# Optimization experiments

Hardware: AMD Instinct MI355X
Metric: run time of the kernel (lower is better)

The kernel has to match this reference:

```python
import jax, jax.numpy as jnp
import numpy as np

B, SIZE_IN, SIZE_OUT = 16384, 256, 4096
NUM_QUANTILES = 32  # boundaries per column = NUM_QUANTILES - 1 = 31


def setup_inputs() -> dict:
    key = jax.random.key(0)
    k1, k2, k3, k4 = jax.random.split(key, 4)
    x = jax.random.normal(k1, (B, SIZE_IN), dtype=jnp.float32)
    weights = jax.random.normal(k2, (SIZE_OUT, SIZE_IN), dtype=jnp.float32) * (1.0 / np.sqrt(SIZE_IN))
    bound = 1.0 / np.sqrt(SIZE_IN)
    bias = jax.random.uniform(k3, (SIZE_OUT,), dtype=jnp.float32, minval=-bound, maxval=bound)
    # per-column quantile boundaries, sorted ascending along last axis
    q = jax.random.normal(k4, (SIZE_OUT, NUM_QUANTILES - 1), dtype=jnp.float32) * np.sqrt(SIZE_IN)
    quantiles = jnp.sort(q, axis=-1)
    return {"x": x, "weights": weights, "bias": bias, "quantiles": quantiles}


def reference(x, weights, bias, quantiles):
    # w_times_x: [B, size_out]
    wx = jnp.matmul(x, weights.T)
    # binarySearchQuantiles: first i with activation <= quantiles[col][i],
    # else len(quantiles[col]) => searchsorted(side='left') per column.
    # quantiles: [size_out, Q-1], wx column j searched against quantiles[j].
    indices = jax.vmap(
        lambda bounds, vals: jnp.searchsorted(bounds, vals, side="left"),
        in_axes=(0, 1), out_axes=1,
    )(quantiles, wx)  # [B, size_out] int32
    out = wx + bias  # broadcast bias over batch
    return out, indices.astype(jnp.float32)
```

## Files before the change

kernel.cpp:

```cpp
#include <hip/hip_runtime.h>


#define B_DIM 16384
#define K_DIM 256
#define N_DIM 4096
#define NQ 31
#define QCAP 2048
#define DELTA 1e-3f

typedef __bf16 bf16x8 __attribute__((ext_vector_type(8)));
typedef float f32x4 __attribute__((ext_vector_type(4)));
typedef unsigned short ushort8 __attribute__((ext_vector_type(8)));

typedef const __attribute__((address_space(1))) unsigned int gu32;
typedef __attribute__((address_space(3))) unsigned int lu32;

__global__ __launch_bounds__(256)
void split_pack(const float* __restrict__ X, const float* __restrict__ W,
                unsigned short* __restrict__ Xhi, unsigned short* __restrict__ Xmid,
                unsigned short* __restrict__ Whi, unsigned short* __restrict__ Wmid)
{
    const int b = blockIdx.x;
    const int tid = threadIdx.x;
    const int r = tid >> 1, ch = tid & 1;

    const float* src;
    unsigned short *dhi, *dmid;
    if (b < 1024) {
        const unsigned u = b;
        src = X + ((size_t)(u >> 3) * 128 + r) * K_DIM + (u & 7) * 32 + ch * 16;
        dhi = Xhi + (size_t)u * 4096; dmid = Xmid + (size_t)u * 4096;
    } else {
        const unsigned u = b - 1024;
        src = W + ((size_t)(u >> 3) * 128 + r) * K_DIM + (u & 7) * 32 + ch * 16;
        dhi = Whi + (size_t)u * 4096; dmid = Wmid + (size_t)u * 4096;
    }

    float4 v0 = *(const float4*)src;
    float4 v1 = *(const float4*)(src + 4);
    float4 v2 = *(const float4*)(src + 8);
    float4 v3 = *(const float4*)(src + 12);
    float xs[16] = {v0.x, v0.y, v0.z, v0.w, v1.x, v1.y, v1.z, v1.w,
                    v2.x, v2.y, v2.z, v2.w, v3.x, v3.y, v3.z, v3.w};
    ushort8 h[2], m[2];
#pragma unroll
    for (int j = 0; j < 16; ++j) {
        float x = xs[j];
        __bf16 hb = (__bf16)x;
        float hf = (float)hb;
        __bf16 mb = (__bf16)(x - hf);
        h[j >> 3][j & 7] = __builtin_bit_cast(unsigned short, hb);
        m[j >> 3][j & 7] = __builtin_bit_cast(unsigned short, mb);
    }
    const unsigned off = (unsigned)(ch * 2) * 1024u + (unsigned)r * 8u;
    *(ushort8*)(dhi + off)         = h[0];
    *(ushort8*)(dhi + off + 1024)  = h[1];
    *(ushort8*)(dmid + off)        = m[0];
    *(ushort8*)(dmid + off + 1024) = m[1];
}

__global__ __launch_bounds__(256)
void eidetic_mfma(const unsigned short* __restrict__ Xhi, const unsigned short* __restrict__ Xmid,
                  const unsigned short* __restrict__ Whi, const unsigned short* __restrict__ Wmid,
                  const float* __restrict__ X, const float* __restrict__ W,
                  const float* __restrict__ bias, const float* __restrict__ Q,
                  float* __restrict__ out, float* __restrict__ idxo)
{
    __shared__ unsigned char smem[65536];
    const int tid = threadIdx.x;
    const int lane = tid & 63;
    const int w = tid >> 6;
    const int wm = w >> 1, wn = w & 1;
    const int l15 = lane & 15, lg = lane >> 4;

    const int bid = blockIdx.x;
    const int swz = ((bid & 7) << 9) | (bid >> 3);
    const int mb = swz >> 5, nb = swz & 31;
    const int m0 = mb << 7, n0 = nb << 7;

    const unsigned short* sbase = (w == 0) ? Xhi : (w == 1) ? Xmid : (w == 2) ? Whi : Wmid;
    const int tb = (w < 2) ? mb : nb;
    const unsigned short* sp = sbase + (size_t)tb * 32768 + (size_t)lane * 8;
    const unsigned ldw = (unsigned)w * 8192u;

    const unsigned aoff = (unsigned)(lg * 128 + wm * 64 + l15) * 16u;
    const unsigned boff = 16384u + (unsigned)(lg * 128 + wn * 64 + l15) * 16u;

    f32x4 acc[4][4];
#pragma unroll
    for (int i = 0; i < 4; ++i)
#pragma unroll
        for (int j = 0; j < 4; ++j) acc[i][j] = (f32x4){0.f, 0.f, 0.f, 0.f};

#pragma unroll
    for (int i = 0; i < 8; ++i)
        __builtin_amdgcn_global_load_lds((gu32*)(sp + i * 512),
                                         (lu32*)(smem + ldw + i * 1024), 16, 0, 0);

    for (int ks = 0; ks < 8; ++ks) {
        __syncthreads();
        if (ks < 7) {
            const unsigned short* s = sp + (ks + 1) * 4096;
            const unsigned bufn = ((unsigned)(ks + 1) & 1u) * 32768u;
#pragma unroll
            for (int i = 0; i < 8; ++i)
                __builtin_amdgcn_global_load_lds((gu32*)(s + i * 512),
                                                 (lu32*)(smem + bufn + ldw + i * 1024), 16, 0, 0);
        }
        const unsigned buf = ((unsigned)ks & 1u) * 32768u;
        bf16x8 ah[4], am[4], bh[4], bm[4];
#pragma unroll
        for (int f = 0; f < 4; ++f) {
            ah[f] = *(const bf16x8*)(smem + buf + aoff + f * 256);
            am[f] = *(const bf16x8*)(smem + buf + 8192u + aoff + f * 256);
            bh[f] = *(const bf16x8*)(smem + buf + boff + f * 256);
            bm[f] = *(const bf16x8*)(smem + buf + 8192u + boff + f * 256);
        }
#pragma unroll
        for (int fi = 0; fi < 4; ++fi)
#pragma unroll
            for (int fj = 0; fj < 4; ++fj) {
                acc[fi][fj] = __builtin_amdgcn_mfma_f32_16x16x32_bf16(ah[fi], bh[fj], acc[fi][fj], 0, 0, 0);
                acc[fi][fj] = __builtin_amdgcn_mfma_f32_16x16x32_bf16(ah[fi], bm[fj], acc[fi][fj], 0, 0, 0);
                acc[fi][fj] = __builtin_amdgcn_mfma_f32_16x16x32_bf16(am[fi], bh[fj], acc[fi][fj], 0, 0, 0);
            }
    }

    float* Qs = (float*)smem;
    {
        const float* qsrc = Q + (size_t)n0 * NQ;
        for (int t = tid; t < 128 * NQ; t += 256) Qs[t] = qsrc[t];
    }
    int* qcnt = (int*)(smem + 15872);
    int* qbuf = qcnt + 1;
    if (tid == 0) *qcnt = 0;
    __syncthreads();

    const int rb = wm * 64 + (lg << 2);

    float bv4[4]; int qb4[4]; int ln4[4];
#pragma unroll
    for (int fj = 0; fj < 4; ++fj) {
        const int ln = wn * 64 + fj * 16 + l15;
        ln4[fj] = ln;
        bv4[fj] = bias[n0 + ln];
        qb4[fj] = ln * NQ;
    }

#pragma unroll
    for (int fi = 0; fi < 4; ++fi) {
#pragma unroll
        for (int r = 0; r < 4; ++r) {
            const int lrow = rb + fi * 16 + r;
            const size_t rowo = (size_t)(m0 + lrow) * N_DIM + n0;
            float ov[4], cv[4];
#pragma unroll
            for (int fj = 0; fj < 4; ++fj) {
                const float v = acc[fi][fj][r];
                const int qb = qb4[fj];
                int c = (Qs[qb + 15] < v) ? 16 : 0;
                c += (Qs[qb + c + 7] < v) ? 8 : 0;
                c += (Qs[qb + c + 3] < v) ? 4 : 0;
                c += (Qs[qb + c + 1] < v) ? 2 : 0;
                c += (Qs[qb + c] < v) ? 1 : 0;
                bool fl = false;
                if (c > 0)  fl = (v - Qs[qb + c - 1]) < DELTA;
                if (c < NQ) fl |= (Qs[qb + c] - v) < DELTA;
                if (fl) {
                    int slot = atomicAdd(qcnt, 1);
                    if (slot < QCAP) qbuf[slot] = (lrow << 7) | ln4[fj];
                }
                ov[fj] = v + bv4[fj];
                cv[fj] = (float)c;
            }
#pragma unroll
            for (int fj = 0; fj < 4; ++fj) out[rowo + ln4[fj]]  = ov[fj];
#pragma unroll
            for (int fj = 0; fj < 4; ++fj) idxo[rowo + ln4[fj]] = cv[fj];
        }
    }

    __syncthreads();
    int tot = *qcnt;
    if (tot > QCAP) tot = QCAP;
    for (int e = tid; e < tot; e += 256) {
        const int pk = qbuf[e];
        const int lm = pk >> 7, lc = pk & 127;
        const float* xr = X + (size_t)(m0 + lm) * K_DIM;
        const float* wr = W + (size_t)(n0 + lc) * K_DIM;
        float a = 0.f;
        for (int k = 0; k < K_DIM; ++k) a = fmaf(xr[k], wr[k], a);
        int c = 0;
        const int qb2 = lc * NQ;
        for (int t = 0; t < NQ; ++t) c += (Qs[qb2 + t] < a) ? 1 : 0;
        const size_t o = (size_t)(m0 + lm) * N_DIM + (n0 + lc);
        out[o] = a + bias[n0 + lc];
        idxo[o] = (float)c;
    }
}

extern "C" void kernel_launch(void* const* d_in, const int* in_sizes, int n_in,
                              void* d_out, int out_size, void* d_ws, size_t ws_size,
                              hipStream_t stream) {
    const float* x    = (const float*)d_in[0];
    const float* wgt  = (const float*)d_in[1];
    const float* bias = (const float*)d_in[2];
    const float* q    = (const float*)d_in[3];
    float* out  = (float*)d_out;
    float* idxo = out + (size_t)B_DIM * N_DIM;

    unsigned short* Xhi  = (unsigned short*)d_ws;
    unsigned short* Xmid = Xhi  + (size_t)B_DIM * K_DIM;
    unsigned short* Whi  = Xmid + (size_t)B_DIM * K_DIM;
    unsigned short* Wmid = Whi  + (size_t)N_DIM * K_DIM;

    hipLaunchKernelGGL(split_pack, dim3(1280), dim3(256), 0, stream,
                       x, wgt, Xhi, Xmid, Whi, Wmid);
    hipLaunchKernelGGL(eidetic_mfma, dim3(4096), dim3(256), 0, stream,
                       Xhi, Xmid, Whi, Wmid, x, wgt, bias, q, out, idxo);
}
```

Measured before the change: 789.3 us.

## Split 128x128 tile across 8 waves instead of 4 in MFMA kernel

Doubles the workgroup to 512 threads so each wave computes a 64x32 sub-tile instead of 64x64, and splits the global-to-LDS staging loads across two waves per operand plane. This halves per-wave accumulator registers and MFMA work, aiming for more waves in flight to hide memory latency during the K loop and the epilogue stores. In exchange, A fragments are reloaded from LDS by more waves, and the 64KB LDS per block still limits how many blocks fit per CU.

```diff
diff --git a/kernel.cpp b/kernel.cpp
--- a/kernel.cpp
+++ b/kernel.cpp
@@ -59,7 +59,7 @@
     *(ushort8*)(dmid + off + 1024) = m[1];
 }
 
-__global__ __launch_bounds__(256)
+__global__ __launch_bounds__(512, 4)
 void eidetic_mfma(const unsigned short* __restrict__ Xhi, const unsigned short* __restrict__ Xmid,
                   const unsigned short* __restrict__ Whi, const unsigned short* __restrict__ Wmid,
                   const float* __restrict__ X, const float* __restrict__ W,
@@ -70,7 +70,7 @@
     const int tid = threadIdx.x;
     const int lane = tid & 63;
     const int w = tid >> 6;
-    const int wm = w >> 1, wn = w & 1;
+    const int wm = w >> 2, wn = w & 3;
     const int l15 = lane & 15, lg = lane >> 4;
 
     const int bid = blockIdx.x;
@@ -78,22 +78,23 @@
     const int mb = swz >> 5, nb = swz & 31;
     const int m0 = mb << 7, n0 = nb << 7;
 
-    const unsigned short* sbase = (w == 0) ? Xhi : (w == 1) ? Xmid : (w == 2) ? Whi : Wmid;
-    const int tb = (w < 2) ? mb : nb;
-    const unsigned short* sp = sbase + (size_t)tb * 32768 + (size_t)lane * 8;
-    const unsigned ldw = (unsigned)w * 8192u;
-
-    const unsigned aoff = (unsigned)(lg * 128 + wm * 64 + l15) * 16u;
-    const unsigned boff = 16384u + (unsigned)(lg * 128 + wn * 64 + l15) * 16u;
-
-    f32x4 acc[4][4];
+    const int p = w >> 1, h = w & 1;
+    const unsigned short* sbase = (p == 0) ? Xhi : (p == 1) ? Xmid : (p == 2) ? Whi : Wmid;
+    const int tb = (p < 2) ? mb : nb;
+    const unsigned short* sp = sbase + (size_t)tb * 32768 + h * 2048 + (size_t)lane * 8;
+    const unsigned ldw = (unsigned)p * 8192u + (unsigned)h * 4096u;
+
+    const unsigned abase = (unsigned)(lg * 128 + wm * 64 + l15) * 16u;
+    const unsigned bbase = 16384u + (unsigned)(lg * 128 + wn * 32 + l15) * 16u;
+
+    f32x4 acc[4][2];
 #pragma unroll
     for (int i = 0; i < 4; ++i)
 #pragma unroll
-        for (int j = 0; j < 4; ++j) acc[i][j] = (f32x4){0.f, 0.f, 0.f, 0.f};
-
-#pragma unroll
-    for (int i = 0; i < 8; ++i)
+        for (int j = 0; j < 2; ++j) acc[i][j] = (f32x4){0.f, 0.f, 0.f, 0.f};
+
+#pragma unroll
+    for (int i = 0; i < 4; ++i)
         __builtin_amdgcn_global_load_lds((gu32*)(sp + i * 512),
                                          (lu32*)(smem + ldw + i * 1024), 16, 0, 0);
 
@@ -103,23 +104,26 @@
             const unsigned short* s = sp + (ks + 1) * 4096;
             const unsigned bufn = ((unsigned)(ks + 1) & 1u) * 32768u;
 #pragma unroll
-            for (int i = 0; i < 8; ++i)
+            for (int i = 0; i < 4; ++i)
                 __builtin_amdgcn_global_load_lds((gu32*)(s + i * 512),
                                                  (lu32*)(smem + bufn + ldw + i * 1024), 16, 0, 0);
         }
         const unsigned buf = ((unsigned)ks & 1u) * 32768u;
-        bf16x8 ah[4], am[4], bh[4], bm[4];
+        bf16x8 ah[4], am[4], bh[2], bm[2];
 #pragma unroll
         for (int f = 0; f < 4; ++f) {
-            ah[f] = *(const bf16x8*)(smem + buf + aoff + f * 256);
-            am[f] = *(const bf16x8*)(smem + buf + 8192u + aoff + f * 256);
-            bh[f] = *(const bf16x8*)(smem + buf + boff + f * 256);
-            bm[f] = *(const bf16x8*)(smem + buf + 8192u + boff + f * 256);
+            ah[f] = *(const bf16x8*)(smem + buf + abase + f * 256);
+            am[f] = *(const bf16x8*)(smem + buf + 8192u + abase + f * 256);
+        }
+#pragma unroll
+        for (int f = 0; f < 2; ++f) {
+            bh[f] = *(const bf16x8*)(smem + buf + bbase + f * 256);
+            bm[f] = *(const bf16x8*)(smem + buf + 8192u + bbase + f * 256);
         }
 #pragma unroll
         for (int fi = 0; fi < 4; ++fi)
 #pragma unroll
-            for (int fj = 0; fj < 4; ++fj) {
+            for (int fj = 0; fj < 2; ++fj) {
                 acc[fi][fj] = __builtin_amdgcn_mfma_f32_16x16x32_bf16(ah[fi], bh[fj], acc[fi][fj], 0, 0, 0);
                 acc[fi][fj] = __builtin_amdgcn_mfma_f32_16x16x32_bf16(ah[fi], bm[fj], acc[fi][fj], 0, 0, 0);
                 acc[fi][fj] = __builtin_amdgcn_mfma_f32_16x16x32_bf16(am[fi], bh[fj], acc[fi][fj], 0, 0, 0);
@@ -129,7 +133,7 @@
     float* Qs = (float*)smem;
     {
         const float* qsrc = Q + (size_t)n0 * NQ;
-        for (int t = tid; t < 128 * NQ; t += 256) Qs[t] = qsrc[t];
+        for (int t = tid; t < 128 * NQ; t += 512) Qs[t] = qsrc[t];
     }
     int* qcnt = (int*)(smem + 15872);
     int* qbuf = qcnt + 1;
@@ -138,13 +142,13 @@
 
     const int rb = wm * 64 + (lg << 2);
 
-    float bv4[4]; int qb4[4]; int ln4[4];
-#pragma unroll
-    for (int fj = 0; fj < 4; ++fj) {
-        const int ln = wn * 64 + fj * 16 + l15;
-        ln4[fj] = ln;
-        bv4[fj] = bias[n0 + ln];
-        qb4[fj] = ln * NQ;
+    float bv2[2]; int qb2[2]; int ln2[2];
+#pragma unroll
+    for (int fj = 0; fj < 2; ++fj) {
+        const int ln = wn * 32 + fj * 16 + l15;
+        ln2[fj] = ln;
+        bv2[fj] = bias[n0 + ln];
+        qb2[fj] = ln * NQ;
     }
 
 #pragma unroll
@@ -153,11 +157,11 @@
         for (int r = 0; r < 4; ++r) {
             const int lrow = rb + fi * 16 + r;
             const size_t rowo = (size_t)(m0 + lrow) * N_DIM + n0;
-            float ov[4], cv[4];
-#pragma unroll
-            for (int fj = 0; fj < 4; ++fj) {
+            float ov[2], cv[2];
+#pragma unroll
+            for (int fj = 0; fj < 2; ++fj) {
                 const float v = acc[fi][fj][r];
-                const int qb = qb4[fj];
+                const int qb = qb2[fj];
                 int c = (Qs[qb + 15] < v) ? 16 : 0;
                 c += (Qs[qb + c + 7] < v) ? 8 : 0;
                 c += (Qs[qb + c + 3] < v) ? 4 : 0;
@@ -168,22 +172,22 @@
                 if (c < NQ) fl |= (Qs[qb + c] - v) < DELTA;
                 if (fl) {
                     int slot = atomicAdd(qcnt, 1);
-                    if (slot < QCAP) qbuf[slot] = (lrow << 7) | ln4[fj];
+                    if (slot < QCAP) qbuf[slot] = (lrow << 7) | ln2[fj];
                 }
-                ov[fj] = v + bv4[fj];
+                ov[fj] = v + bv2[fj];
                 cv[fj] = (float)c;
             }
 #pragma unroll
-            for (int fj = 0; fj < 4; ++fj) out[rowo + ln4[fj]]  = ov[fj];
-#pragma unroll
-            for (int fj = 0; fj < 4; ++fj) idxo[rowo + ln4[fj]] = cv[fj];
+            for (int fj = 0; fj < 2; ++fj) out[rowo + ln2[fj]]  = ov[fj];
+#pragma unroll
+            for (int fj = 0; fj < 2; ++fj) idxo[rowo + ln2[fj]] = cv[fj];
         }
     }
 
     __syncthreads();
     int tot = *qcnt;
     if (tot > QCAP) tot = QCAP;
-    for (int e = tid; e < tot; e += 256) {
+    for (int e = tid; e < tot; e += 512) {
         const int pk = qbuf[e];
         const int lm = pk >> 7, lc = pk & 127;
         const float* xr = X + (size_t)(m0 + lm) * K_DIM;
@@ -191,8 +195,8 @@
         float a = 0.f;
         for (int k = 0; k < K_DIM; ++k) a = fmaf(xr[k], wr[k], a);
         int c = 0;
-        const int qb2 = lc * NQ;
-        for (int t = 0; t < NQ; ++t) c += (Qs[qb2 + t] < a) ? 1 : 0;
+        const int qb2s = lc * NQ;
+        for (int t = 0; t < NQ; ++t) c += (Qs[qb2s + t] < a) ? 1 : 0;
         const size_t o = (size_t)(m0 + lm) * N_DIM + (n0 + lc);
         out[o] = a + bias[n0 + lc];
         idxo[o] = (float)c;
@@ -216,6 +220,6 @@
 
     hipLaunchKernelGGL(split_pack, dim3(1280), dim3(256), 0, stream,
                        x, wgt, Xhi, Xmid, Whi, Wmid);
-    hipLaunchKernelGGL(eidetic_mfma, dim3(4096), dim3(256), 0, stream,
+    hipLaunchKernelGGL(eidetic_mfma, dim3(4096), dim3(512), 0, stream,
                        Xhi, Xmid, Whi, Wmid, x, wgt, bias, q, out, idxo);
 }
```

Result: faster. 716.0 us (-9.3%).
